# Kernel optimization log

Hardware: AMD Instinct MI355X
Metric: run time of the kernel (lower is better)

The kernel has to match this reference:

```python
import jax, jax.numpy as jnp
import numpy as np

H = 4  # fixed number of heads in the layer


def setup_inputs() -> dict:
    key = jax.random.key(0)
    ks = jax.random.split(key, 6)
    B, S, D = 4, 2048, 512
    U = 2 * D  # per-head projection width (units = d_model * 2)
    x = jax.random.normal(ks[0], (B, S, D), dtype=jnp.float32)
    gamma = jnp.ones((D,), dtype=jnp.float32)
    beta = jnp.zeros((D,), dtype=jnp.float32)
    s = 0.02
    Wq = jax.random.normal(ks[1], (H, D, U), dtype=jnp.float32) * s
    Wk = jax.random.normal(ks[2], (H, D, U), dtype=jnp.float32) * s
    Wv = jax.random.normal(ks[3], (H, D, U), dtype=jnp.float32) * s
    Wout = jax.random.normal(ks[4], (H * U, D), dtype=jnp.float32) * s
    return {"x": x, "gamma": gamma, "beta": beta, "Wq": Wq, "Wk": Wk, "Wv": Wv, "Wout": Wout}


def _forward(x, gamma, beta, Wq, Wk, Wv, Wout):
    B, S, D = x.shape
    eps = 1e-6
    # LayerNormalization over last axis (Keras default, eps=1e-6)
    mu = jnp.mean(x, axis=-1, keepdims=True)
    var = jnp.mean(jnp.square(x - mu), axis=-1, keepdims=True)
    xn = (x - mu) * jax.lax.rsqrt(var + eps) * gamma + beta
    # Per-head Q/K/V projections, batched over head axis. Dropout is identity at inference.
    q = jnp.einsum('bsd,hdu->bhsu', xn, Wq)
    k = jnp.einsum('bsd,hdu->bhsu', xn, Wk)
    v = jnp.einsum('bsd,hdu->bhsu', xn, Wv)
    # Keras Attention(use_scale=False, causal=True): unscaled dot-product scores
    scores = jnp.einsum('bhsu,bhtu->bhst', q, k)  # [B,H,S,S]
    causal = jnp.tril(jnp.ones((S, S), dtype=bool))
    scores = jnp.where(causal, scores, jnp.finfo(scores.dtype).min)
    probs = jax.nn.softmax(scores, axis=-1)
    head = jnp.einsum('bhst,bhtu->bhsu', probs, v)  # [B,H,S,U]
    # concat heads in head order -> [B,S,H*U], then output Dense back to D
    HU = head.shape[1] * head.shape[3]
    cat = head.transpose(0, 2, 1, 3).reshape(B, S, HU)
    return cat @ Wout


def reference(x, gamma, beta, Wq, Wk, Wv, Wout):
    return _forward(x, gamma, beta, Wq, Wk, Wv, Wout)
```

## Files before the change

kernel.cpp:

```cpp
#include <hip/hip_runtime.h>

typedef _Float16 half8 __attribute__((ext_vector_type(8)));
typedef float floatx4 __attribute__((ext_vector_type(4)));

__device__ __forceinline__ void gl16(const _Float16* g, _Float16* l) {
    __builtin_amdgcn_global_load_lds((const __attribute__((address_space(1))) void*)g,
                                     (__attribute__((address_space(3))) void*)l, 16, 0, 0);
}

__global__ __launch_bounds__(64) void ln_k(const float* __restrict__ x,
                                           const float* __restrict__ gamma,
                                           const float* __restrict__ beta,
                                           _Float16* __restrict__ xn) {
    const int D = 512;
    long long base = (long long)blockIdx.x * D;
    int lane = threadIdx.x;
    floatx4 x0 = *(const floatx4*)(x + base + lane * 8);
    floatx4 x1 = *(const floatx4*)(x + base + lane * 8 + 4);
    float f[8];
#pragma unroll
    for (int i = 0; i < 4; i++) { f[i] = x0[i]; f[4 + i] = x1[i]; }
    float s = 0.f, ss = 0.f;
#pragma unroll
    for (int i = 0; i < 8; i++) { s += f[i]; ss += f[i] * f[i]; }
#pragma unroll
    for (int off = 32; off; off >>= 1) { s += __shfl_xor(s, off); ss += __shfl_xor(ss, off); }
    float mean = s * (1.f / 512.f);
    float var = ss * (1.f / 512.f) - mean * mean;
    float rstd = rsqrtf(var + 1e-6f);
    floatx4 g0 = *(const floatx4*)(gamma + lane * 8);
    floatx4 g1 = *(const floatx4*)(gamma + lane * 8 + 4);
    floatx4 b0 = *(const floatx4*)(beta + lane * 8);
    floatx4 b1 = *(const floatx4*)(beta + lane * 8 + 4);
    half8 o;
#pragma unroll
    for (int i = 0; i < 4; i++) {
        o[i]     = (_Float16)((f[i]     - mean) * rstd * g0[i] + b0[i]);
        o[4 + i] = (_Float16)((f[4 + i] - mean) * rstd * g1[i] + b1[i]);
    }
    *(half8*)(xn + base + lane * 8) = o;
}

__global__ __launch_bounds__(256) void tr_k(const float* __restrict__ in,
                                            _Float16* __restrict__ out, int R, int C) {
    __shared__ _Float16 tile[32][33];
    int tx = threadIdx.x, ty = threadIdx.y;
    long long zo = (long long)blockIdx.z * R * C;
    int r0 = blockIdx.y * 32, c0 = blockIdx.x * 32;
    for (int yy = ty; yy < 32; yy += 8)
        tile[yy][tx] = (_Float16)in[zo + (long long)(r0 + yy) * C + c0 + tx];
    __syncthreads();
    for (int yy = ty; yy < 32; yy += 8)
        out[zo + (long long)(c0 + yy) * R + r0 + tx] = tile[tx][yy];
}

#define BM 128
#define BN 128
#define BK 32
__global__ __launch_bounds__(256) void gemm_bt(
    const _Float16* __restrict__ A, const _Float16* __restrict__ Bt, void* __restrict__ Cv,
    int K, int ldc, int cflags,
    int dA, int mA, long long sA, int dB, int mB, long long sB, long long sC) {
    int z = blockIdx.z;
    const _Float16* Ab = A + (long long)((z / dA) % mA) * sA;
    const _Float16* Bb = Bt + (long long)((z / dB) % mB) * sB;
    long long offC = (long long)z * sC;

    int gx = gridDim.x, gy = gridDim.y;
    int nb = gx * gy;
    int lin = blockIdx.y * gx + blockIdx.x;
    int mIdx, nIdx;
    if (((nb & 7) == 0) && ((gx & 3) == 0)) {
        int chunk = nb >> 3;
        int vid = (lin >> 3) + chunk * (lin & 7);
        int panelH = gy * 4;
        int panel = vid / panelH;
        int rem = vid - panel * panelH;
        mIdx = rem >> 2;
        nIdx = (panel << 2) + (rem & 3);
    } else { mIdx = blockIdx.y; nIdx = blockIdx.x; }
    int m0 = mIdx * BM, n0 = nIdx * BN;

    if ((cflags & 4) && n0 > m0 + (BM - 1)) return;
    int kend = (cflags & 8) ? min(K, m0 + BM) : K;

    __shared__ _Float16 As[2][BM * BK];
    __shared__ _Float16 Bs[2][BN * BK];

    int t = threadIdx.x;
    int srow = t >> 2;
    int scol = (t & 3) * 8;
    int lane = t & 63, w = t >> 6;
    int wm = (w >> 1) * 64, wn = (w & 1) * 64;
    int lm = lane & 15, lk = (lane >> 4) * 8;

    floatx4 acc[4][4];
#pragma unroll
    for (int i = 0; i < 4; i++)
#pragma unroll
        for (int j = 0; j < 4; j++) acc[i][j] = floatx4{0.f, 0.f, 0.f, 0.f};

    const _Float16* ga0 = Ab + (long long)(m0 + srow) * K + scol;
    const _Float16* ga1 = Ab + (long long)(m0 + 64 + srow) * K + scol;
    const _Float16* gb0 = Bb + (long long)(n0 + srow) * K + scol;
    const _Float16* gb1 = Bb + (long long)(n0 + 64 + srow) * K + scol;

    int nIter = kend / BK;
    gl16(ga0, &As[0][t * 8]);
    gl16(ga1, &As[0][2048 + t * 8]);
    gl16(gb0, &Bs[0][t * 8]);
    gl16(gb1, &Bs[0][2048 + t * 8]);

    for (int it = 0; it < nIter; it++) {
        __syncthreads();
        int cur = it & 1;
        half8 af[4], bfr[4];
#pragma unroll
        for (int i = 0; i < 4; i++) af[i] = *(const half8*)&As[cur][(wm + i * 16 + lm) * BK + lk];
#pragma unroll
        for (int j = 0; j < 4; j++) bfr[j] = *(const half8*)&Bs[cur][(wn + j * 16 + lm) * BK + lk];
        if (it + 1 < nIter) {
            int nk = (it + 1) * BK;
            int nxt = cur ^ 1;
            gl16(ga0 + nk, &As[nxt][t * 8]);
            gl16(ga1 + nk, &As[nxt][2048 + t * 8]);
            gl16(gb0 + nk, &Bs[nxt][t * 8]);
            gl16(gb1 + nk, &Bs[nxt][2048 + t * 8]);
        }
#pragma unroll
        for (int i = 0; i < 4; i++)
#pragma unroll
            for (int j = 0; j < 4; j++)
                acc[i][j] = __builtin_amdgcn_mfma_f32_16x16x32_f16(af[i], bfr[j], acc[i][j], 0, 0, 0);
    }

    int cr = (lane >> 4) * 4;
    int cc = lm;
    bool outf32 = (cflags & 1) != 0;
#pragma unroll
    for (int i = 0; i < 4; i++) {
#pragma unroll
        for (int j = 0; j < 4; j++) {
            int rr = m0 + wm + i * 16 + cr;
            int nn = n0 + wn + j * 16 + cc;
#pragma unroll
            for (int r2 = 0; r2 < 4; r2++) {
                long long idx = (long long)(rr + r2) * ldc + nn + offC;
                float val = acc[i][j][r2];
                if (outf32) ((float*)Cv)[idx] = val;
                else ((_Float16*)Cv)[idx] = (_Float16)val;
            }
        }
    }
}

__global__ __launch_bounds__(256) void softmax_h(_Float16* __restrict__ sc, int S) {
    int wid = threadIdx.x >> 6, lane = threadIdx.x & 63;
    int idx = blockIdx.x * 4 + wid;
    int r = idx & (S - 1);
    _Float16* srow = sc + (long long)idx * S;
    int nc = r >> 9;
    float v[32];
    float mx = -3.0e38f;
    for (int c = 0; c <= nc; c++) {
        half8 hv = *(half8*)(srow + lane * 8 + c * 512);
#pragma unroll
        for (int i = 0; i < 8; i++) {
            int n = lane * 8 + c * 512 + i;
            float s = (n <= r) ? (float)hv[i] : -3.0e38f;
            v[c * 8 + i] = s; mx = fmaxf(mx, s);
        }
    }
#pragma unroll
    for (int off = 32; off; off >>= 1) mx = fmaxf(mx, __shfl_xor(mx, off));
    float sum = 0.f;
    for (int c = 0; c <= nc; c++)
#pragma unroll
        for (int i = 0; i < 8; i++) {
            int n = lane * 8 + c * 512 + i;
            float e = (n <= r) ? __expf(v[c * 8 + i] - mx) : 0.f;
            v[c * 8 + i] = e; sum += e;
        }
#pragma unroll
    for (int off = 32; off; off >>= 1) sum += __shfl_xor(sum, off);
    float inv = 1.f / sum;
    for (int c = 0; c <= nc; c++) {
        half8 o;
#pragma unroll
        for (int i = 0; i < 8; i++) o[i] = (_Float16)(v[c * 8 + i] * inv);
        *(half8*)(srow + lane * 8 + c * 512) = o;
    }
}

extern "C" void kernel_launch(void* const* d_in, const int* in_sizes, int n_in,
                              void* d_out, int out_size, void* d_ws, size_t ws_size,
                              hipStream_t stream) {
    const int B = 4, S = 2048, D = 512, H = 4, U = 1024;
    const float* x     = (const float*)d_in[0];
    const float* gamma = (const float*)d_in[1];
    const float* beta  = (const float*)d_in[2];
    const float* Wq    = (const float*)d_in[3];
    const float* Wk    = (const float*)d_in[4];
    const float* Wv    = (const float*)d_in[5];
    const float* Wout  = (const float*)d_in[6];
    float* out = (float*)d_out;

    char* ws = (char*)d_ws;
    const size_t MiB = 1ull << 20;
    const long long SD = (long long)S * D, UD = (long long)U * D;
    const long long SU = (long long)S * U, SS = (long long)S * S, US = (long long)U * S;
    const long long HU = (long long)H * U;

    _Float16* xn  = (_Float16*)(ws + 0);
    _Float16* WqT = (_Float16*)(ws + 8  * MiB);
    _Float16* WkT = (_Float16*)(ws + 12 * MiB);
    _Float16* WvT = (_Float16*)(ws + 16 * MiB);
    _Float16* WoT = (_Float16*)(ws + 20 * MiB);

    tr_k<<<dim3(U / 32, D / 32, H), dim3(32, 8), 0, stream>>>(Wq, WqT, D, U);
    tr_k<<<dim3(U / 32, D / 32, H), dim3(32, 8), 0, stream>>>(Wk, WkT, D, U);
    tr_k<<<dim3(U / 32, D / 32, H), dim3(32, 8), 0, stream>>>(Wv, WvT, D, U);
    tr_k<<<dim3(D / 32, (H * U) / 32, 1), dim3(32, 8), 0, stream>>>(Wout, WoT, H * U, D);
    ln_k<<<B * S, 64, 0, stream>>>(x, gamma, beta, xn);

    if (ws_size >= 168 * MiB) {
        _Float16* qb  = (_Float16*)(ws + 24  * MiB);
        _Float16* kb  = (_Float16*)(ws + 40  * MiB);
        _Float16* vTb = (_Float16*)(ws + 56  * MiB);
        _Float16* sc  = (_Float16*)(ws + 72  * MiB);
        _Float16* cat = (_Float16*)(ws + 104 * MiB);

        for (int b = 0; b < B; b++) {
            const _Float16* xnb = xn + (long long)b * SD;
            gemm_bt<<<dim3(U / 128, S / 128, 2 * H), 256, 0, stream>>>(xnb, WqT, qb, D, U, 0,
                1, 1, 0, 1, 2 * H, UD, SU);
            gemm_bt<<<dim3(S / 128, U / 128, H), 256, 0, stream>>>(WvT, xnb, vTb, D, S, 0,
                1, H, UD, 1, 1, 0, US);
            gemm_bt<<<dim3(S / 128, S / 128, H), 256, 0, stream>>>(qb, kb, sc, U, S, 4,
                1, H, SU, 1, H, SU, SS);
            softmax_h<<<H * S / 4, 256, 0, stream>>>(sc, S);
            gemm_bt<<<dim3(U / 128, S / 128, H), 256, 0, stream>>>(sc, vTb,
                (void*)(cat + (long long)b * S * HU), S, H * U, 8,
                1, H, SS, 1, H, US, U);
        }
        gemm_bt<<<dim3(D / 128, (B * S) / 128, 1), 256, 0, stream>>>(cat, WoT, out,
            H * U, D, 1, 1, 1, 0, 1, 1, 0, 0);
    } else {
        _Float16* qb   = (_Float16*)(ws + 24 * MiB);
        _Float16* kb   = (_Float16*)(ws + 40 * MiB);
        _Float16* vTb  = (_Float16*)(ws + 56 * MiB);
        _Float16* catb = (_Float16*)(ws + 72 * MiB);
        _Float16* sc   = (_Float16*)(ws + 88 * MiB);

        for (int b = 0; b < B; b++) {
            const _Float16* xnb = xn + (long long)b * SD;
            gemm_bt<<<dim3(U / 128, S / 128, 2 * H), 256, 0, stream>>>(xnb, WqT, qb, D, U, 0,
                1, 1, 0, 1, 2 * H, UD, SU);
            gemm_bt<<<dim3(S / 128, U / 128, H), 256, 0, stream>>>(WvT, xnb, vTb, D, S, 0,
                1, H, UD, 1, 1, 0, US);
            for (int h = 0; h < H; h++) {
                gemm_bt<<<dim3(S / 128, S / 128, 1), 256, 0, stream>>>(qb + (long long)h * SU,
                    kb + (long long)h * SU, sc, U, S, 4, 1, 1, 0, 1, 1, 0, 0);
                softmax_h<<<S / 4, 256, 0, stream>>>(sc, S);
                gemm_bt<<<dim3(U / 128, S / 128, 1), 256, 0, stream>>>(sc,
                    vTb + (long long)h * US, (void*)(catb + (long long)h * U), S, H * U, 8,
                    1, 1, 0, 1, 1, 0, 0);
            }
            gemm_bt<<<dim3(D / 128, S / 128, 1), 256, 0, stream>>>(catb, WoT,
                (void*)(out + (long long)b * SD), H * U, D, 1, 1, 1, 0, 1, 1, 0, 0);
        }
    }
}
```

Before: 744.3 us.

## Batch two sequences per launch and reuse workspace buffers across stages

The main path now processes two batch elements per group of launches instead of one. That doubles the grid z-dimension for the QK projection, scores, softmax, V projection and PV GEMMs, and the output projection runs per pair. Generic div/mod stride arithmetic is replaced with a compile-time switch on a mode argument. The V-transpose and concat buffers alias the Q/K region, so the V projection is reordered to run after the scores. The aim is to cut launch count and raise occupancy per launch, at the cost of a larger score buffer and more complex aliasing.

```diff
diff --git a/kernel.cpp b/kernel.cpp
--- a/kernel.cpp
+++ b/kernel.cpp
@@ -7,6 +7,17 @@
     __builtin_amdgcn_global_load_lds((const __attribute__((address_space(1))) void*)g,
                                      (__attribute__((address_space(3))) void*)l, 16, 0, 0);
 }
+
+#define Scst 2048
+#define Dcst 512
+#define Ucst 1024
+#define Hcst 4
+#define SDo 1048576LL
+#define UDo 524288LL
+#define SUo 2097152LL
+#define SSo 4194304LL
+#define USo 2097152LL
+#define SHUo 8388608LL
 
 __global__ __launch_bounds__(64) void ln_k(const float* __restrict__ x,
                                            const float* __restrict__ gamma,
@@ -59,12 +70,36 @@
 #define BK 32
 __global__ __launch_bounds__(256) void gemm_bt(
     const _Float16* __restrict__ A, const _Float16* __restrict__ Bt, void* __restrict__ Cv,
-    int K, int ldc, int cflags,
-    int dA, int mA, long long sA, int dB, int mB, long long sB, long long sC) {
+    int K, int ldc, int cflags, int mode) {
     int z = blockIdx.z;
-    const _Float16* Ab = A + (long long)((z / dA) % mA) * sA;
-    const _Float16* Bb = Bt + (long long)((z / dB) % mB) * sB;
-    long long offC = (long long)z * sC;
+    long long offA = 0, offB = 0, offC = 0;
+    switch (mode) {
+        case 1:
+            offA = (long long)((z >> 2) & 1) * SDo;
+            offB = (long long)(((z >> 3) * 4) + (z & 3)) * UDo;
+            offC = (long long)(((z >> 3) * 8) + ((z & 3) * 2) + ((z >> 2) & 1)) * SUo;
+            break;
+        case 2:
+            offA = (long long)z * SUo; offB = (long long)z * SUo; offC = (long long)z * SSo;
+            break;
+        case 3:
+            offA = (long long)(z >> 1) * UDo; offB = (long long)(z & 1) * SDo;
+            offC = (long long)z * USo;
+            break;
+        case 4:
+            offA = (long long)z * SSo; offB = (long long)z * USo;
+            offC = (long long)(z & 1) * SHUo + (long long)(z >> 1) * Ucst;
+            break;
+        case 6:
+            offB = (long long)(z & 7) * UDo; offC = (long long)z * SUo;
+            break;
+        case 7:
+            offA = (long long)(z & 3) * UDo; offC = (long long)z * USo;
+            break;
+        default: break;
+    }
+    const _Float16* Ab = A + offA;
+    const _Float16* Bb = Bt + offB;
 
     int gx = gridDim.x, gy = gridDim.y;
     int nb = gx * gy;
@@ -207,9 +242,7 @@
 
     char* ws = (char*)d_ws;
     const size_t MiB = 1ull << 20;
-    const long long SD = (long long)S * D, UD = (long long)U * D;
-    const long long SU = (long long)S * U, SS = (long long)S * S, US = (long long)U * S;
-    const long long HU = (long long)H * U;
+    const long long SD = SDo, UD = UDo, SU = SUo, US = USo;
 
     _Float16* xn  = (_Float16*)(ws + 0);
     _Float16* WqT = (_Float16*)(ws + 8  * MiB);
@@ -224,50 +257,42 @@
     ln_k<<<B * S, 64, 0, stream>>>(x, gamma, beta, xn);
 
     if (ws_size >= 168 * MiB) {
-        _Float16* qb  = (_Float16*)(ws + 24  * MiB);
-        _Float16* kb  = (_Float16*)(ws + 40  * MiB);
-        _Float16* vTb = (_Float16*)(ws + 56  * MiB);
-        _Float16* sc  = (_Float16*)(ws + 72  * MiB);
-        _Float16* cat = (_Float16*)(ws + 104 * MiB);
-
-        for (int b = 0; b < B; b++) {
-            const _Float16* xnb = xn + (long long)b * SD;
-            gemm_bt<<<dim3(U / 128, S / 128, 2 * H), 256, 0, stream>>>(xnb, WqT, qb, D, U, 0,
-                1, 1, 0, 1, 2 * H, UD, SU);
-            gemm_bt<<<dim3(S / 128, U / 128, H), 256, 0, stream>>>(WvT, xnb, vTb, D, S, 0,
-                1, H, UD, 1, 1, 0, US);
-            gemm_bt<<<dim3(S / 128, S / 128, H), 256, 0, stream>>>(qb, kb, sc, U, S, 4,
-                1, H, SU, 1, H, SU, SS);
-            softmax_h<<<H * S / 4, 256, 0, stream>>>(sc, S);
-            gemm_bt<<<dim3(U / 128, S / 128, H), 256, 0, stream>>>(sc, vTb,
-                (void*)(cat + (long long)b * S * HU), S, H * U, 8,
-                1, H, SS, 1, H, US, U);
-        }
-        gemm_bt<<<dim3(D / 128, (B * S) / 128, 1), 256, 0, stream>>>(cat, WoT, out,
-            H * U, D, 1, 1, 1, 0, 1, 1, 0, 0);
+        _Float16* qk  = (_Float16*)(ws + 24 * MiB);
+        _Float16* kk  = qk + 8 * SU;
+        _Float16* sc  = (_Float16*)(ws + 88 * MiB);
+        _Float16* vt  = qk;
+        _Float16* cat = kk;
+
+        for (int p = 0; p < 2; p++) {
+            const _Float16* xnp = xn + (long long)p * 2 * SD;
+            float* outp = out + (long long)p * 2 * SD;
+            gemm_bt<<<dim3(U / 128, S / 128, 16), 256, 0, stream>>>(xnp, WqT, qk, D, U, 0, 1);
+            gemm_bt<<<dim3(S / 128, S / 128, 8), 256, 0, stream>>>(qk, kk, sc, U, S, 4, 2);
+            softmax_h<<<8 * S / 4, 256, 0, stream>>>(sc, S);
+            gemm_bt<<<dim3(S / 128, U / 128, 8), 256, 0, stream>>>(WvT, xnp, vt, D, S, 0, 3);
+            gemm_bt<<<dim3(U / 128, S / 128, 8), 256, 0, stream>>>(sc, vt, cat, S, H * U, 8, 4);
+            gemm_bt<<<dim3(D / 128, 2 * S / 128, 1), 256, 0, stream>>>(cat, WoT, outp,
+                H * U, D, 1, 0);
+        }
     } else {
         _Float16* qb   = (_Float16*)(ws + 24 * MiB);
-        _Float16* kb   = (_Float16*)(ws + 40 * MiB);
         _Float16* vTb  = (_Float16*)(ws + 56 * MiB);
         _Float16* catb = (_Float16*)(ws + 72 * MiB);
         _Float16* sc   = (_Float16*)(ws + 88 * MiB);
 
         for (int b = 0; b < B; b++) {
             const _Float16* xnb = xn + (long long)b * SD;
-            gemm_bt<<<dim3(U / 128, S / 128, 2 * H), 256, 0, stream>>>(xnb, WqT, qb, D, U, 0,
-                1, 1, 0, 1, 2 * H, UD, SU);
-            gemm_bt<<<dim3(S / 128, U / 128, H), 256, 0, stream>>>(WvT, xnb, vTb, D, S, 0,
-                1, H, UD, 1, 1, 0, US);
+            gemm_bt<<<dim3(U / 128, S / 128, 2 * H), 256, 0, stream>>>(xnb, WqT, qb, D, U, 0, 6);
+            gemm_bt<<<dim3(S / 128, U / 128, H), 256, 0, stream>>>(WvT, xnb, vTb, D, S, 0, 7);
             for (int h = 0; h < H; h++) {
                 gemm_bt<<<dim3(S / 128, S / 128, 1), 256, 0, stream>>>(qb + (long long)h * SU,
-                    kb + (long long)h * SU, sc, U, S, 4, 1, 1, 0, 1, 1, 0, 0);
+                    qb + (long long)(H + h) * SU, sc, U, S, 4, 0);
                 softmax_h<<<S / 4, 256, 0, stream>>>(sc, S);
                 gemm_bt<<<dim3(U / 128, S / 128, 1), 256, 0, stream>>>(sc,
-                    vTb + (long long)h * US, (void*)(catb + (long long)h * U), S, H * U, 8,
-                    1, 1, 0, 1, 1, 0, 0);
+                    vTb + (long long)h * US, (void*)(catb + (long long)h * U), S, H * U, 8, 0);
             }
             gemm_bt<<<dim3(D / 128, S / 128, 1), 256, 0, stream>>>(catb, WoT,
-                (void*)(out + (long long)b * SD), H * U, D, 1, 1, 1, 0, 1, 1, 0, 0);
-        }
-    }
-}
+                (void*)(out + (long long)b * SD), H * U, D, 1, 0);
+        }
+    }
+}
```

Result: no change. 742.6 us (-0.2%).
